# Optimization experiments

Hardware: AMD Instinct MI355X
Metric: run time of the kernel (lower is better)

Reference implementation:

```python
import jax, jax.numpy as jnp
import numpy as np

LN_EPS = 1e-5  # torch LayerNorm default


def setup_inputs() -> dict:
    key = jax.random.key(0)
    k1, k2, k3 = jax.random.split(key, 3)
    B, L, D = 8, 2048, 1024
    CS, CD = 8192, 16
    x = jax.random.normal(k1, (B, L, D), dtype=jnp.float32)
    # xavier_uniform for Linear(dim, codebook_dim): bound = sqrt(6/(fan_in+fan_out))
    bound = float(np.sqrt(6.0 / (D + CD)))
    W = jax.random.uniform(k2, (CD, D), dtype=jnp.float32, minval=-bound, maxval=bound)
    codebook = jax.random.normal(k3, (CS, CD), dtype=jnp.float32)
    return {"x": x, "W": W, "codebook": codebook}


def reference(x, W, codebook):
    # random projection: (B,L,D) @ (D,CD) -> (B,L,CD)
    z = jnp.einsum("bld,cd->blc", x, W)
    # LayerNorm over last dim, no affine
    mu = jnp.mean(z, axis=-1, keepdims=True)
    var = jnp.mean(jnp.square(z - mu), axis=-1, keepdims=True)
    z = (z - mu) / jnp.sqrt(var + LN_EPS)
    # squared euclidean distance via matmul decomposition (avoids (B,L,CS,CD) tensor):
    # ||z - c||^2 = ||z||^2 - 2 z.c + ||c||^2 ; argmin is identical to argmin of the norm
    z_sq = jnp.sum(jnp.square(z), axis=-1, keepdims=True)        # (B,L,1)
    c_sq = jnp.sum(jnp.square(codebook), axis=-1)                # (CS,)
    d2 = z_sq - 2.0 * jnp.einsum("blc,kc->blk", z, codebook) + c_sq  # (B,L,CS)
    codes = jnp.argmin(d2, axis=-1)                              # (B,L) int32
    return codes
```

## Files before the change

kernel.cpp:

```cpp
#include <hip/hip_runtime.h>
#include <math.h>

#define D      1024
#define CD     16
#define CS     8192
#define ROWS   16384
#define LN_EPS 1e-5f
#define KCHUNK 512
#define NCHUNK (CS / KCHUNK)

typedef __attribute__((ext_vector_type(8))) short short8;
typedef __attribute__((ext_vector_type(4))) float f32x4;

__device__ inline unsigned short bf16_rne(float v) {
    unsigned u = __float_as_uint(v);
    unsigned r = u + 0x7FFFu + ((u >> 16) & 1u);
    return (unsigned short)(r >> 16);
}
__device__ inline short8 ld8(const unsigned short* p) { return *(const short8*)p; }

__device__ inline void split3(float v, unsigned short& a, unsigned short& b, unsigned short& c) {
    unsigned u = __float_as_uint(v);
    unsigned r = u + 0x7FFFu + ((u >> 16) & 1u);
    a = (unsigned short)(r >> 16);
    float r1 = v - __uint_as_float(r & 0xFFFF0000u);
    unsigned u1 = __float_as_uint(r1);
    unsigned r1b = u1 + 0x7FFFu + ((u1 >> 16) & 1u);
    b = (unsigned short)(r1b >> 16);
    float r2 = r1 - __uint_as_float(r1b & 0xFFFF0000u);
    c = bf16_rne(r2);
}

__global__ __launch_bounds__(256) void pack_all(const float* __restrict__ W,
                                                const float* __restrict__ cb,
                                                unsigned short* __restrict__ wb,
                                                unsigned short* __restrict__ bstream,
                                                float* __restrict__ nhc)
{
    const int t = threadIdx.x;
    const int b = blockIdx.x;
    if (b < 32) {
        int k = b * 256 + t;
        const float* c = cb + (long)k * CD;
        float csq = 0.f;
        #pragma unroll
        for (int d = 0; d < 16; ++d) csq = fmaf(c[d], c[d], csq);
        nhc[k] = -0.5f * csq;
    } else if (b < 288) {
        int gid = (b - 32) * 256 + t;
        int L = gid & 63;
        int g = (gid >> 6) & 1;
        int T = gid >> 7;
        int n = L & 15, q = L >> 4;
        int k = T * 16 + n;
        int o = (g == 0) ? q * 8 : (q < 2 ? q * 8 : 16 + q * 8);
        int term = o >> 4;
        int d0 = o & 15;
        const float* c = cb + (long)k * CD + d0;
        unsigned short out[8];
        #pragma unroll
        for (int j = 0; j < 8; ++j) {
            unsigned short h0, h1, h2;
            split3(c[j], h0, h1, h2);
            out[j] = term == 0 ? h0 : (term == 1 ? h1 : h2);
        }
        *(short8*)(bstream + (size_t)gid * 8) = *(short8*)out;
    } else {
        int tid = (b - 288) * 256 + t;
        int gk   = tid / 192;
        int rem  = tid % 192;
        int term = rem >> 6;
        int L    = rem & 63;
        int n = L & 15, q = L >> 4;
        const float* src = W + n * D + gk * 32 + q * 8;
        unsigned short* dst = wb + (size_t)tid * 8;
        #pragma unroll
        for (int j = 0; j < 8; ++j) {
            unsigned short h0, h1, h2;
            split3(src[j], h0, h1, h2);
            dst[j] = term == 0 ? h0 : (term == 1 ? h1 : h2);
        }
    }
}

__global__ __launch_bounds__(256, 4) void proj_ln(const float* __restrict__ x,
                                                  const unsigned short* __restrict__ wb,
                                                  unsigned short* __restrict__ zp)
{
    __shared__ float part[3][64][4];
    const int t = threadIdx.x;
    const int L = t & 63;
    const int kq = t >> 6;
    const int rt = blockIdx.x;
    const int n = L & 15, q = L >> 4;

    const float* xrow = x + (size_t)(rt * 16 + n) * D + kq * 256 + q * 8;
    const unsigned short* wbase = wb + (size_t)(kq * 8) * 1536;

    f32x4 acc0 = {0.f, 0.f, 0.f, 0.f};
    f32x4 acc1 = {0.f, 0.f, 0.f, 0.f};
    #pragma unroll
    for (int kk = 0; kk < 8; ++kk) {
        float4 xa = *(const float4*)(xrow + kk * 32);
        float4 xb = *(const float4*)(xrow + kk * 32 + 4);
        const unsigned short* wp = wbase + (size_t)kk * 1536 + L * 8;
        short8 w0 = ld8(wp);
        short8 w1 = ld8(wp + 512);
        short8 w2 = ld8(wp + 1024);
        float vs[8] = {xa.x, xa.y, xa.z, xa.w, xb.x, xb.y, xb.z, xb.w};
        short8 x0, x1, x2;
        #pragma unroll
        for (int j = 0; j < 8; ++j) {
            unsigned short h0, h1, h2;
            split3(vs[j], h0, h1, h2);
            x0[j] = (short)h0; x1[j] = (short)h1; x2[j] = (short)h2;
        }
        acc0 = __builtin_amdgcn_mfma_f32_16x16x32_bf16(x0, w0, acc0, 0, 0, 0);
        acc1 = __builtin_amdgcn_mfma_f32_16x16x32_bf16(x0, w1, acc1, 0, 0, 0);
        acc0 = __builtin_amdgcn_mfma_f32_16x16x32_bf16(x1, w0, acc0, 0, 0, 0);
        acc1 = __builtin_amdgcn_mfma_f32_16x16x32_bf16(x1, w1, acc1, 0, 0, 0);
        acc0 = __builtin_amdgcn_mfma_f32_16x16x32_bf16(x0, w2, acc0, 0, 0, 0);
        acc1 = __builtin_amdgcn_mfma_f32_16x16x32_bf16(x2, w0, acc1, 0, 0, 0);
    }

    if (kq != 0) {
        #pragma unroll
        for (int r = 0; r < 4; ++r) part[kq - 1][L][r] = acc0[r] + acc1[r];
    }
    __syncthreads();
    if (kq == 0) {
        #pragma unroll
        for (int r = 0; r < 4; ++r) {
            float zv = acc0[r] + acc1[r] + part[0][L][r] + part[1][L][r] + part[2][L][r];
            float s = zv;
            for (int m = 1; m < 16; m <<= 1) s += __shfl_xor(s, m, 64);
            float mu = s * (1.f / 16.f);
            float dd = zv - mu;
            float v2 = dd * dd;
            for (int m = 1; m < 16; m <<= 1) v2 += __shfl_xor(v2, m, 64);
            float var = v2 * (1.f / 16.f);
            float zn = dd / sqrtf(var + LN_EPS);
            unsigned short h0, h1, h2;
            split3(zn, h0, h1, h2);
            unsigned short* zr = zp + (size_t)(rt * 16 + q * 4 + r) * 48;
            zr[n] = h0; zr[16 + n] = h1; zr[32 + n] = h2;
        }
    }
}

__global__ __launch_bounds__(256, 4) void dist_argmin(const unsigned short* __restrict__ zp,
                                                      const unsigned short* __restrict__ bstream,
                                                      const float* __restrict__ nhc,
                                                      float* __restrict__ pbest,
                                                      int* __restrict__ pidx)
{
    const int t = threadIdx.x;
    const int L = t & 63;
    const int w = t >> 6;
    const int n = L & 15;
    const int q = L >> 4;
    const int kbase = blockIdx.y * KCHUNK;
    const int Tbase = kbase >> 4;

    const short8* bs = (const short8*)bstream + (size_t)Tbase * 128 + L;

    const int oa2 = (q * 8 + 16) & 31;
    const int oa3 = q < 2 ? 32 + q * 8 : (q - 2) * 8;

    short8 a1[4], a2[4], a3[4];
    const int rt0 = blockIdx.x * 16 + w * 4;
    #pragma unroll
    for (int j = 0; j < 4; ++j) {
        const unsigned short* zr = zp + (size_t)((rt0 + j) * 16 + n) * 48;
        a1[j] = ld8(zr + q * 8);
        a2[j] = ld8(zr + oa2);
        a3[j] = ld8(zr + oa3);
    }

    float best[4][4];
    int   bi[4][4];
    #pragma unroll
    for (int j = 0; j < 4; ++j)
        #pragma unroll
        for (int r = 0; r < 4; ++r) { best[j][r] = -INFINITY; bi[j][r] = 0; }

    short8 b1n = bs[0];
    short8 b3n = bs[64];
    float  qn  = nhc[kbase + n];

    for (int tt = 0; tt < KCHUNK / 16; ++tt) {
        short8 b1 = b1n, b3 = b3n;
        float qv = qn;
        if (tt + 1 < KCHUNK / 16) {
            b1n = bs[(tt + 1) * 128];
            b3n = bs[(tt + 1) * 128 + 64];
            qn  = nhc[kbase + (tt + 1) * 16 + n];
        }
        f32x4 bias = {qv, qv, qv, qv};
        int code = kbase + tt * 16 + n;
        #pragma unroll
        for (int j = 0; j < 4; ++j) {
            f32x4 acc;
            acc = __builtin_amdgcn_mfma_f32_16x16x32_bf16(a1[j], b1, bias, 0, 0, 0);
            acc = __builtin_amdgcn_mfma_f32_16x16x32_bf16(a2[j], b1, acc, 0, 0, 0);
            acc = __builtin_amdgcn_mfma_f32_16x16x32_bf16(a3[j], b3, acc, 0, 0, 0);
            #pragma unroll
            for (int r = 0; r < 4; ++r)
                if (acc[r] > best[j][r]) { best[j][r] = acc[r]; bi[j][r] = code; }
        }
    }

    #pragma unroll
    for (int mask = 1; mask < 16; mask <<= 1) {
        #pragma unroll
        for (int j = 0; j < 4; ++j)
            #pragma unroll
            for (int r = 0; r < 4; ++r) {
                float s2 = __shfl_xor(best[j][r], mask, 64);
                int   i2 = __shfl_xor(bi[j][r], mask, 64);
                if (s2 > best[j][r] || (s2 == best[j][r] && i2 < bi[j][r])) {
                    best[j][r] = s2; bi[j][r] = i2;
                }
            }
    }
    if (n == 0) {
        #pragma unroll
        for (int j = 0; j < 4; ++j)
            #pragma unroll
            for (int r = 0; r < 4; ++r) {
                int row = (rt0 + j) * 16 + q * 4 + r;
                pbest[(size_t)row * NCHUNK + blockIdx.y] = best[j][r];
                pidx [(size_t)row * NCHUNK + blockIdx.y] = bi[j][r];
            }
    }
}

__global__ __launch_bounds__(256) void merge_argmin(const float* __restrict__ pbest,
                                                    const int* __restrict__ pidx,
                                                    int* __restrict__ out)
{
    const long row = (long)blockIdx.x * 256 + threadIdx.x;
    float best = -INFINITY;
    int   bi   = 0;
    #pragma unroll
    for (int i = 0; i < NCHUNK; ++i) {
        float s = pbest[row * NCHUNK + i];
        if (s > best) { best = s; bi = pidx[row * NCHUNK + i]; }
    }
    out[row] = bi;
}

extern "C" void kernel_launch(void* const* d_in, const int* in_sizes, int n_in,
                              void* d_out, int out_size, void* d_ws, size_t ws_size,
                              hipStream_t stream)
{
    const float* x  = (const float*)d_in[0];
    const float* W  = (const float*)d_in[1];
    const float* cb = (const float*)d_in[2];
    int* out = (int*)d_out;

    char* ws = (char*)d_ws;
    unsigned short* zp  = (unsigned short*)ws;
    float* nhc  = (float*)(ws + 0x180000);
    unsigned short* wb = (unsigned short*)(ws + 0x188000);
    unsigned short* bstream = (unsigned short*)(ws + 0x1A0000);
    float* pbest = (float*)(ws + 0x2A0000);
    int*   pidx  = (int*)  (ws + 0x3A0000);

    pack_all<<<312, 256, 0, stream>>>(W, cb, wb, bstream, nhc);
    proj_ln <<<ROWS / 16, 256, 0, stream>>>(x, wb, zp);
    dist_argmin<<<dim3(ROWS / 256, NCHUNK), 256, 0, stream>>>(zp, bstream, nhc, pbest, pidx);
    merge_argmin<<<ROWS / 256, 256, 0, stream>>>(pbest, pidx, out);
}
```

Measured before the change: 140.9 us.

## Switch distance kernel to 32x32x16 MFMA tiles with two accumulator chains

Repacks the codebook into a 32-code bf16x3 stream and rewrites dist_argmin to use 32x32x16 MFMA instructions. Each wave now handles 32 rows against 32 codes per step, with two independent accumulators (bias plus main terms, and cross terms) summed before the argmin compare. This cuts the number of argmin compare passes per MFMA FLOP and shrinks the packed codebook layout. In exchange it uses more accumulator registers per wave and doubles the grid's x dimension, and it has a 32-lane reduction whose row-index mapping must match the 32x32 output layout.

```diff
diff --git a/kernel.cpp b/kernel.cpp
--- a/kernel.cpp
+++ b/kernel.cpp
@@ -9,8 +9,9 @@
 #define KCHUNK 512
 #define NCHUNK (CS / KCHUNK)
 
-typedef __attribute__((ext_vector_type(8))) short short8;
-typedef __attribute__((ext_vector_type(4))) float f32x4;
+typedef __attribute__((ext_vector_type(8)))  short short8;
+typedef __attribute__((ext_vector_type(4)))  float f32x4;
+typedef __attribute__((ext_vector_type(16))) float f32x16;
 
 __device__ inline unsigned short bf16_rne(float v) {
     unsigned u = __float_as_uint(v);
@@ -34,7 +35,7 @@
 __global__ __launch_bounds__(256) void pack_all(const float* __restrict__ W,
                                                 const float* __restrict__ cb,
                                                 unsigned short* __restrict__ wb,
-                                                unsigned short* __restrict__ bstream,
+                                                unsigned short* __restrict__ bs32,
                                                 float* __restrict__ nhc)
 {
     const int t = threadIdx.x;
@@ -46,27 +47,24 @@
         #pragma unroll
         for (int d = 0; d < 16; ++d) csq = fmaf(c[d], c[d], csq);
         nhc[k] = -0.5f * csq;
-    } else if (b < 288) {
+    } else if (b < 224) {
         int gid = (b - 32) * 256 + t;
         int L = gid & 63;
-        int g = (gid >> 6) & 1;
-        int T = gid >> 7;
-        int n = L & 15, q = L >> 4;
-        int k = T * 16 + n;
-        int o = (g == 0) ? q * 8 : (q < 2 ? q * 8 : 16 + q * 8);
-        int term = o >> 4;
-        int d0 = o & 15;
+        int s = (gid >> 6) % 3;
+        int T = gid / 192;
+        int k = T * 32 + (L & 31);
+        int d0 = (L >> 5) * 8;
         const float* c = cb + (long)k * CD + d0;
         unsigned short out[8];
         #pragma unroll
         for (int j = 0; j < 8; ++j) {
             unsigned short h0, h1, h2;
             split3(c[j], h0, h1, h2);
-            out[j] = term == 0 ? h0 : (term == 1 ? h1 : h2);
-        }
-        *(short8*)(bstream + (size_t)gid * 8) = *(short8*)out;
+            out[j] = s == 0 ? h0 : (s == 1 ? h1 : h2);
+        }
+        *(short8*)(bs32 + (size_t)gid * 8) = *(short8*)out;
     } else {
-        int tid = (b - 288) * 256 + t;
+        int tid = (b - 224) * 256 + t;
         int gk   = tid / 192;
         int rem  = tid % 192;
         int term = rem >> 6;
@@ -149,7 +147,7 @@
 }
 
 __global__ __launch_bounds__(256, 4) void dist_argmin(const unsigned short* __restrict__ zp,
-                                                      const unsigned short* __restrict__ bstream,
+                                                      const unsigned short* __restrict__ bs32,
                                                       const float* __restrict__ nhc,
                                                       float* __restrict__ pbest,
                                                       int* __restrict__ pidx)
@@ -157,81 +155,68 @@
     const int t = threadIdx.x;
     const int L = t & 63;
     const int w = t >> 6;
-    const int n = L & 15;
-    const int q = L >> 4;
+    const int n = L & 31;
+    const int h = L >> 5;
     const int kbase = blockIdx.y * KCHUNK;
-    const int Tbase = kbase >> 4;
-
-    const short8* bs = (const short8*)bstream + (size_t)Tbase * 128 + L;
-
-    const int oa2 = (q * 8 + 16) & 31;
-    const int oa3 = q < 2 ? 32 + q * 8 : (q - 2) * 8;
-
-    short8 a1[4], a2[4], a3[4];
-    const int rt0 = blockIdx.x * 16 + w * 4;
-    #pragma unroll
-    for (int j = 0; j < 4; ++j) {
-        const unsigned short* zr = zp + (size_t)((rt0 + j) * 16 + n) * 48;
-        a1[j] = ld8(zr + q * 8);
-        a2[j] = ld8(zr + oa2);
-        a3[j] = ld8(zr + oa3);
-    }
-
-    float best[4][4];
-    int   bi[4][4];
-    #pragma unroll
-    for (int j = 0; j < 4; ++j)
-        #pragma unroll
-        for (int r = 0; r < 4; ++r) { best[j][r] = -INFINITY; bi[j][r] = 0; }
-
-    short8 b1n = bs[0];
-    short8 b3n = bs[64];
-    float  qn  = nhc[kbase + n];
-
-    for (int tt = 0; tt < KCHUNK / 16; ++tt) {
-        short8 b1 = b1n, b3 = b3n;
-        float qv = qn;
-        if (tt + 1 < KCHUNK / 16) {
-            b1n = bs[(tt + 1) * 128];
-            b3n = bs[(tt + 1) * 128 + 64];
-            qn  = nhc[kbase + (tt + 1) * 16 + n];
-        }
-        f32x4 bias = {qv, qv, qv, qv};
-        int code = kbase + tt * 16 + n;
-        #pragma unroll
-        for (int j = 0; j < 4; ++j) {
-            f32x4 acc;
-            acc = __builtin_amdgcn_mfma_f32_16x16x32_bf16(a1[j], b1, bias, 0, 0, 0);
-            acc = __builtin_amdgcn_mfma_f32_16x16x32_bf16(a2[j], b1, acc, 0, 0, 0);
-            acc = __builtin_amdgcn_mfma_f32_16x16x32_bf16(a3[j], b3, acc, 0, 0, 0);
-            #pragma unroll
-            for (int r = 0; r < 4; ++r)
-                if (acc[r] > best[j][r]) { best[j][r] = acc[r]; bi[j][r] = code; }
-        }
-    }
-
-    #pragma unroll
-    for (int mask = 1; mask < 16; mask <<= 1) {
-        #pragma unroll
-        for (int j = 0; j < 4; ++j)
-            #pragma unroll
-            for (int r = 0; r < 4; ++r) {
-                float s2 = __shfl_xor(best[j][r], mask, 64);
-                int   i2 = __shfl_xor(bi[j][r], mask, 64);
-                if (s2 > best[j][r] || (s2 == best[j][r] && i2 < bi[j][r])) {
-                    best[j][r] = s2; bi[j][r] = i2;
-                }
+
+    const int row0 = (blockIdx.x * 4 + w) * 32;
+    const unsigned short* zr = zp + (size_t)(row0 + n) * 48 + h * 8;
+    short8 a0 = ld8(zr);
+    short8 a1 = ld8(zr + 16);
+    short8 a2 = ld8(zr + 32);
+
+    const short8* bs = (const short8*)bs32 + (size_t)(blockIdx.y * 16) * 192 + L;
+
+    f32x16 ZERO;
+    #pragma unroll
+    for (int r = 0; r < 16; ++r) ZERO[r] = 0.f;
+
+    float best[16];
+    int   bi[16];
+    #pragma unroll
+    for (int r = 0; r < 16; ++r) { best[r] = -INFINITY; bi[r] = 0; }
+
+    #pragma unroll 2
+    for (int tt = 0; tt < KCHUNK / 32; ++tt) {
+        short8 b0 = bs[tt * 192];
+        short8 b1 = bs[tt * 192 + 64];
+        short8 b2 = bs[tt * 192 + 128];
+        float qv = nhc[kbase + tt * 32 + n];
+        f32x16 accA;
+        #pragma unroll
+        for (int r = 0; r < 16; ++r) accA[r] = qv;
+        accA = __builtin_amdgcn_mfma_f32_32x32x16_bf16(a0, b0, accA, 0, 0, 0);
+        f32x16 accB = __builtin_amdgcn_mfma_f32_32x32x16_bf16(a0, b1, ZERO, 0, 0, 0);
+        accA = __builtin_amdgcn_mfma_f32_32x32x16_bf16(a1, b0, accA, 0, 0, 0);
+        accB = __builtin_amdgcn_mfma_f32_32x32x16_bf16(a1, b1, accB, 0, 0, 0);
+        accA = __builtin_amdgcn_mfma_f32_32x32x16_bf16(a2, b0, accA, 0, 0, 0);
+        accB = __builtin_amdgcn_mfma_f32_32x32x16_bf16(a0, b2, accB, 0, 0, 0);
+        int code = kbase + tt * 32 + n;
+        #pragma unroll
+        for (int r = 0; r < 16; ++r) {
+            float s = accA[r] + accB[r];
+            if (s > best[r]) { best[r] = s; bi[r] = code; }
+        }
+    }
+
+    #pragma unroll
+    for (int mask = 1; mask < 32; mask <<= 1) {
+        #pragma unroll
+        for (int r = 0; r < 16; ++r) {
+            float s2 = __shfl_xor(best[r], mask, 64);
+            int   i2 = __shfl_xor(bi[r], mask, 64);
+            if (s2 > best[r] || (s2 == best[r] && i2 < bi[r])) {
+                best[r] = s2; bi[r] = i2;
             }
+        }
     }
     if (n == 0) {
         #pragma unroll
-        for (int j = 0; j < 4; ++j)
-            #pragma unroll
-            for (int r = 0; r < 4; ++r) {
-                int row = (rt0 + j) * 16 + q * 4 + r;
-                pbest[(size_t)row * NCHUNK + blockIdx.y] = best[j][r];
-                pidx [(size_t)row * NCHUNK + blockIdx.y] = bi[j][r];
-            }
+        for (int r = 0; r < 16; ++r) {
+            int row = row0 + (r & 3) + 8 * (r >> 2) + 4 * h;
+            pbest[(size_t)row * NCHUNK + blockIdx.y] = best[r];
+            pidx [(size_t)row * NCHUNK + blockIdx.y] = bi[r];
+        }
     }
 }
 
@@ -260,15 +245,15 @@
     int* out = (int*)d_out;
 
     char* ws = (char*)d_ws;
-    unsigned short* zp  = (unsigned short*)ws;
+    unsigned short* zp   = (unsigned short*)ws;
     float* nhc  = (float*)(ws + 0x180000);
-    unsigned short* wb = (unsigned short*)(ws + 0x188000);
-    unsigned short* bstream = (unsigned short*)(ws + 0x1A0000);
-    float* pbest = (float*)(ws + 0x2A0000);
-    int*   pidx  = (int*)  (ws + 0x3A0000);
-
-    pack_all<<<312, 256, 0, stream>>>(W, cb, wb, bstream, nhc);
+    unsigned short* wb   = (unsigned short*)(ws + 0x188000);
+    unsigned short* bs32 = (unsigned short*)(ws + 0x1A0000);
+    float* pbest = (float*)(ws + 0x260000);
+    int*   pidx  = (int*)  (ws + 0x360000);
+
+    pack_all<<<248, 256, 0, stream>>>(W, cb, wb, bs32, nhc);
     proj_ln <<<ROWS / 16, 256, 0, stream>>>(x, wb, zp);
-    dist_argmin<<<dim3(ROWS / 256, NCHUNK), 256, 0, stream>>>(zp, bstream, nhc, pbest, pidx);
+    dist_argmin<<<dim3(ROWS / 128, NCHUNK), 256, 0, stream>>>(zp, bs32, nhc, pbest, pidx);
     merge_argmin<<<ROWS / 256, 256, 0, stream>>>(pbest, pidx, out);
 }
```

Result: slower. 154.8 us (+9.9%).
